# Kernel optimization log

Hardware: AMD Instinct MI355X
Metric: run time of the kernel (lower is better)

## Reference

```python
import jax, jax.numpy as jnp
import numpy as np

IGNORE_INDEX = 255
NUM_CLASSES = 19


def setup_inputs() -> dict:
    key = jax.random.key(0)
    k1, k2 = jax.random.split(key)
    logits = jax.random.normal(k1, (8, NUM_CLASSES, 512, 1024), dtype=jnp.float32)
    labels = jax.random.randint(k2, (8, 512, 1024), 0, NUM_CLASSES, dtype=jnp.int64)
    return {"logits": logits, "labels": labels}


def _lovasz_per_class(err, fg, valid):
    # err, fg, valid: [N] for one class. Sort by error descending.
    order = jnp.argsort(-err)
    es = err[order]
    fs = fg[order]
    vs = valid[order]
    gts = fs.sum()
    intersection = gts - jnp.cumsum(fs)
    # invalid (ignored) pixels contribute to neither fg nor background: vs - fs
    union = gts + jnp.cumsum(vs - fs)
    safe_union = jnp.where(union == 0, 1.0, union)
    jaccard = 1.0 - intersection / safe_union
    grad = jnp.concatenate([jaccard[:1], jaccard[1:] - jaccard[:-1]])
    loss_c = jnp.dot(es, grad)
    present = (gts > 0).astype(es.dtype)
    return loss_c, present


def reference(logits, labels):
    B, C, H, W = logits.shape
    probs = jax.nn.softmax(logits, axis=1)
    probs = probs.transpose(0, 2, 3, 1).reshape(-1, C)  # [N, C]
    lab = labels.reshape(-1)
    valid = (lab != IGNORE_INDEX).astype(probs.dtype)  # [N]
    # one-hot foreground per class, zeroed at ignored pixels
    fg = (lab[:, None] == jnp.arange(C)[None, :]).astype(probs.dtype) * valid[:, None]
    # errors; ignored pixels get error 0 so they sort to the end and contribute 0
    errors = jnp.abs(fg - probs) * valid[:, None]  # [N, C]
    loss_c, present = jax.vmap(_lovasz_per_class, in_axes=(1, 1, None))(errors, fg, valid)
    n_present = jnp.maximum(present.sum(), 1.0)
    return jnp.sum(loss_c * present) / n_present
```

## Files before the change

kernel.cpp:

```cpp
#include <hip/hip_runtime.h>


#define NCLS 19
#define IGNORE_IDX 255

constexpr int HW = 512 * 1024;
constexpr int HW4 = HW / 4;
constexpr int NQUAD = 8 * HW4;
constexpr int NBINS = 512;
constexpr int HSLOTS = NCLS * NBINS;

template <int NHB>
__global__ __launch_bounds__(256) void lovasz_hist(
    const float* __restrict__ logits,
    const int*   __restrict__ labels,
    unsigned int* __restrict__ partial)
{
    constexpr int QPB = NQUAD / NHB;
    constexpr int QPT = QPB / 256;
    __shared__ unsigned int lh[HSLOTS];
    const int t = threadIdx.x;
    for (int i = t; i < HSLOTS; i += 256) lh[i] = 0;
    __syncthreads();

    for (int k = 0; k < QPT; ++k) {
        const int q   = blockIdx.x * QPB + k * 256 + t;
        const int b   = q >> 17;
        const int hw4 = q & (HW4 - 1);
        const float* base = logits + (size_t)b * NCLS * HW + (size_t)hw4 * 4;

        float4 l[NCLS];
        float mx = -3.4e38f, my = -3.4e38f, mz = -3.4e38f, mw = -3.4e38f;
#pragma unroll
        for (int c = 0; c < NCLS; ++c) {
            l[c] = *(const float4*)(base + (size_t)c * HW);
            mx = fmaxf(mx, l[c].x); my = fmaxf(my, l[c].y);
            mz = fmaxf(mz, l[c].z); mw = fmaxf(mw, l[c].w);
        }
        float dx = 0.f, dy = 0.f, dz = 0.f, dw = 0.f;
#pragma unroll
        for (int c = 0; c < NCLS; ++c) {
            l[c].x = __expf(l[c].x - mx); dx += l[c].x;
            l[c].y = __expf(l[c].y - my); dy += l[c].y;
            l[c].z = __expf(l[c].z - mz); dz += l[c].z;
            l[c].w = __expf(l[c].w - mw); dw += l[c].w;
        }
        dx = 1.f / dx; dy = 1.f / dy; dz = 1.f / dz; dw = 1.f / dw;

        const int4 lab = *(const int4*)(labels + (size_t)q * 4);

        auto upd = [&](int c, float p, int lb) {
            if (lb == IGNORE_IDX) return;
            const bool fg = (lb == c);
            const float e = fg ? (1.0f - p) : p;
            int bin = (int)(e * (float)NBINS);
            bin = bin < 0 ? 0 : (bin > NBINS - 1 ? NBINS - 1 : bin);
            atomicAdd(&lh[c * NBINS + bin], fg ? 0x10001u : 1u);
        };
#pragma unroll
        for (int c = 0; c < NCLS; ++c) {
            upd(c, l[c].x * dx, lab.x);
            upd(c, l[c].y * dy, lab.y);
            upd(c, l[c].z * dz, lab.z);
            upd(c, l[c].w * dw, lab.w);
        }
    }
    __syncthreads();
    unsigned int* dst = partial + (size_t)blockIdx.x * HSLOTS;
    for (int i = t; i < HSLOTS; i += 256) dst[i] = lh[i];
}

__global__ __launch_bounds__(256) void lovasz_scan(
    const unsigned int* __restrict__ partial,
    int nhb,
    float* __restrict__ lp)
{
    const int c = blockIdx.x;
    const int t = threadIdx.x;

    unsigned int v0 = 0, g0 = 0, v1 = 0, g1 = 0;
    {
        const unsigned int* p0 = partial + c * NBINS + (NBINS - 2 - 2 * t);
        for (int b = 0; b < nhb; ++b) {
            const uint2 x = *(const uint2*)(p0 + (size_t)b * HSLOTS);
            v0 += x.y & 0xFFFFu; g0 += x.y >> 16;
            v1 += x.x & 0xFFFFu; g1 += x.x >> 16;
        }
    }

    __shared__ unsigned int av[NBINS], ag[NBINS];
    av[2 * t] = v0; ag[2 * t] = g0;
    av[2 * t + 1] = v1; ag[2 * t + 1] = g1;

    __shared__ unsigned int pg[257], pv[257];
    pg[t + 1] = g0 + g1; pv[t + 1] = v0 + v1;
    __syncthreads();
    if (t == 0) {
        pg[0] = 0; pv[0] = 0;
        for (int i = 1; i <= 256; ++i) { pg[i] += pg[i - 1]; pv[i] += pv[i - 1]; }
    }
    __syncthreads();
    const unsigned int G = pg[256];

    double acc = 0.0;
    if (G > 0) {
        unsigned int CF = pg[t], CV = pv[t];
#pragma unroll
        for (int i = 0; i < 2; ++i) {
            const int j = 2 * t + i;
            const int bin = NBINS - 1 - j;
            const unsigned int v = av[j], g = ag[j];
            if (v) {
                const float e  = ((float)bin + 0.5f) * (1.0f / (float)NBINS);
                const float U0 = (float)(G - CF + CV);
                if (g) acc += (double)(e * (float)g / U0);
                const unsigned int nbg = v - g;
                if (nbg) {
                    const float I1 = (float)(G - CF - g);
                    acc += (double)(e * I1 * (float)nbg / (U0 * (U0 + (float)nbg)));
                }
                CF += g; CV += v;
            }
        }
    }

    __shared__ double sacc[256];
    sacc[t] = acc;
    __syncthreads();
    for (int s = 128; s > 0; s >>= 1) {
        if (t < s) sacc[t] += sacc[t + s];
        __syncthreads();
    }
    if (t == 0) {
        lp[c] = (float)sacc[0];
        lp[NCLS + c] = (G > 0) ? 1.0f : 0.0f;
    }
}

__global__ void lovasz_final(const float* __restrict__ lp, float* __restrict__ out) {
    if (threadIdx.x == 0) {
        float s = 0.f, np = 0.f;
        for (int c = 0; c < NCLS; ++c) { s += lp[c] * lp[NCLS + c]; np += lp[NCLS + c]; }
        out[0] = s / fmaxf(np, 1.0f);
    }
}

extern "C" void kernel_launch(void* const* d_in, const int* in_sizes, int n_in,
                              void* d_out, int out_size, void* d_ws, size_t ws_size,
                              hipStream_t stream) {
    const float* logits = (const float*)d_in[0];
    const int*   labels = (const int*)d_in[1];
    float* out = (float*)d_out;

    unsigned int* partial = (unsigned int*)d_ws;
    const size_t need512 = (size_t)512 * HSLOTS * sizeof(unsigned int) + 64 * sizeof(float);

    if (ws_size >= need512) {
        float* lp = (float*)(partial + (size_t)512 * HSLOTS);
        lovasz_hist<512><<<512, 256, 0, stream>>>(logits, labels, partial);
        lovasz_scan<<<NCLS, 256, 0, stream>>>(partial, 512, lp);
        lovasz_final<<<1, 64, 0, stream>>>(lp, out);
    } else {
        float* lp = (float*)(partial + (size_t)256 * HSLOTS);
        lovasz_hist<256><<<256, 256, 0, stream>>>(logits, labels, partial);
        lovasz_scan<<<NCLS, 256, 0, stream>>>(partial, 256, lp);
        lovasz_final<<<1, 64, 0, stream>>>(lp, out);
    }
}
```

Baseline: 525.2 us.

## Halve histogram bins, replicate LDS histograms, drop softmax max pass

Reduces histogram bins from 512 to 256 and keeps four padded copies of the per-block LDS histogram, selected by thread index, to spread atomic contention; the copies are summed on write-out. Softmax drops the max-subtraction pass and uses a hardware reciprocal with the bin scale folded in, cutting ALU work and register pressure. The scan kernel is simplified to one bin per thread with an unrolled partial-sum loop. The changes risk overflow for large logits, coarser loss quantisation, and more LDS use per block, which may lower occupancy.

```diff
diff --git a/kernel.cpp b/kernel.cpp
--- a/kernel.cpp
+++ b/kernel.cpp
@@ -7,8 +7,18 @@
 constexpr int HW = 512 * 1024;
 constexpr int HW4 = HW / 4;
 constexpr int NQUAD = 8 * HW4;
-constexpr int NBINS = 512;
+constexpr int NBINS = 256;
 constexpr int HSLOTS = NCLS * NBINS;
+constexpr int PSTRIDE = HSLOTS + 1;
+constexpr int NCOPY = 4;
+
+__device__ __forceinline__ float fast_rcp(float x) {
+#if defined(__has_builtin) && __has_builtin(__builtin_amdgcn_rcpf)
+    return __builtin_amdgcn_rcpf(x);
+#else
+    return 1.0f / x;
+#endif
+}
 
 template <int NHB>
 __global__ __launch_bounds__(256) void lovasz_hist(
@@ -18,10 +28,12 @@
 {
     constexpr int QPB = NQUAD / NHB;
     constexpr int QPT = QPB / 256;
-    __shared__ unsigned int lh[HSLOTS];
+    __shared__ unsigned int lh[NCOPY * PSTRIDE];
     const int t = threadIdx.x;
-    for (int i = t; i < HSLOTS; i += 256) lh[i] = 0;
+    for (int i = t; i < NCOPY * PSTRIDE; i += 256) lh[i] = 0;
     __syncthreads();
+
+    unsigned int* my = lh + (t & (NCOPY - 1)) * PSTRIDE;
 
     for (int k = 0; k < QPT; ++k) {
         const int q   = blockIdx.x * QPB + k * 256 + t;
@@ -29,45 +41,43 @@
         const int hw4 = q & (HW4 - 1);
         const float* base = logits + (size_t)b * NCLS * HW + (size_t)hw4 * 4;
 
-        float4 l[NCLS];
-        float mx = -3.4e38f, my = -3.4e38f, mz = -3.4e38f, mw = -3.4e38f;
-#pragma unroll
-        for (int c = 0; c < NCLS; ++c) {
-            l[c] = *(const float4*)(base + (size_t)c * HW);
-            mx = fmaxf(mx, l[c].x); my = fmaxf(my, l[c].y);
-            mz = fmaxf(mz, l[c].z); mw = fmaxf(mw, l[c].w);
-        }
+        float ex[NCLS], ey[NCLS], ez[NCLS], ew[NCLS];
         float dx = 0.f, dy = 0.f, dz = 0.f, dw = 0.f;
 #pragma unroll
         for (int c = 0; c < NCLS; ++c) {
-            l[c].x = __expf(l[c].x - mx); dx += l[c].x;
-            l[c].y = __expf(l[c].y - my); dy += l[c].y;
-            l[c].z = __expf(l[c].z - mz); dz += l[c].z;
-            l[c].w = __expf(l[c].w - mw); dw += l[c].w;
+            const float4 l = *(const float4*)(base + (size_t)c * HW);
+            ex[c] = __expf(l.x); dx += ex[c];
+            ey[c] = __expf(l.y); dy += ey[c];
+            ez[c] = __expf(l.z); dz += ez[c];
+            ew[c] = __expf(l.w); dw += ew[c];
         }
-        dx = 1.f / dx; dy = 1.f / dy; dz = 1.f / dz; dw = 1.f / dw;
+        const float rx = (float)NBINS * fast_rcp(dx);
+        const float ry = (float)NBINS * fast_rcp(dy);
+        const float rz = (float)NBINS * fast_rcp(dz);
+        const float rw = (float)NBINS * fast_rcp(dw);
 
         const int4 lab = *(const int4*)(labels + (size_t)q * 4);
 
-        auto upd = [&](int c, float p, int lb) {
+        auto upd = [&](int c, float psc, int lb) {
             if (lb == IGNORE_IDX) return;
             const bool fg = (lb == c);
-            const float e = fg ? (1.0f - p) : p;
-            int bin = (int)(e * (float)NBINS);
-            bin = bin < 0 ? 0 : (bin > NBINS - 1 ? NBINS - 1 : bin);
-            atomicAdd(&lh[c * NBINS + bin], fg ? 0x10001u : 1u);
+            const float bs = fg ? ((float)NBINS - psc) : psc;
+            int bin = (int)bs;
+            bin = bin > NBINS - 1 ? NBINS - 1 : bin;
+            atomicAdd(&my[c * NBINS + bin], fg ? 0x10001u : 1u);
         };
 #pragma unroll
         for (int c = 0; c < NCLS; ++c) {
-            upd(c, l[c].x * dx, lab.x);
-            upd(c, l[c].y * dy, lab.y);
-            upd(c, l[c].z * dz, lab.z);
-            upd(c, l[c].w * dw, lab.w);
+            upd(c, ex[c] * rx, lab.x);
+            upd(c, ey[c] * ry, lab.y);
+            upd(c, ez[c] * rz, lab.z);
+            upd(c, ew[c] * rw, lab.w);
         }
     }
     __syncthreads();
     unsigned int* dst = partial + (size_t)blockIdx.x * HSLOTS;
-    for (int i = t; i < HSLOTS; i += 256) dst[i] = lh[i];
+    for (int i = t; i < HSLOTS; i += 256)
+        dst[i] = lh[i] + lh[i + PSTRIDE] + lh[i + 2 * PSTRIDE] + lh[i + 3 * PSTRIDE];
 }
 
 __global__ __launch_bounds__(256) void lovasz_scan(
@@ -78,22 +88,26 @@
     const int c = blockIdx.x;
     const int t = threadIdx.x;
 
-    unsigned int v0 = 0, g0 = 0, v1 = 0, g1 = 0;
+    unsigned int v = 0, g = 0;
     {
-        const unsigned int* p0 = partial + c * NBINS + (NBINS - 2 - 2 * t);
-        for (int b = 0; b < nhb; ++b) {
-            const uint2 x = *(const uint2*)(p0 + (size_t)b * HSLOTS);
-            v0 += x.y & 0xFFFFu; g0 += x.y >> 16;
-            v1 += x.x & 0xFFFFu; g1 += x.x >> 16;
+        const unsigned int* p0 = partial + c * NBINS + (NBINS - 1 - t);
+        int b = 0;
+        for (; b + 4 <= nhb; b += 4) {
+            const unsigned int x0 = p0[(size_t)(b + 0) * HSLOTS];
+            const unsigned int x1 = p0[(size_t)(b + 1) * HSLOTS];
+            const unsigned int x2 = p0[(size_t)(b + 2) * HSLOTS];
+            const unsigned int x3 = p0[(size_t)(b + 3) * HSLOTS];
+            v += (x0 & 0xFFFFu) + (x1 & 0xFFFFu) + (x2 & 0xFFFFu) + (x3 & 0xFFFFu);
+            g += (x0 >> 16) + (x1 >> 16) + (x2 >> 16) + (x3 >> 16);
+        }
+        for (; b < nhb; ++b) {
+            const unsigned int x = p0[(size_t)b * HSLOTS];
+            v += x & 0xFFFFu; g += x >> 16;
         }
     }
 
-    __shared__ unsigned int av[NBINS], ag[NBINS];
-    av[2 * t] = v0; ag[2 * t] = g0;
-    av[2 * t + 1] = v1; ag[2 * t + 1] = g1;
-
     __shared__ unsigned int pg[257], pv[257];
-    pg[t + 1] = g0 + g1; pv[t + 1] = v0 + v1;
+    pg[t + 1] = g; pv[t + 1] = v;
     __syncthreads();
     if (t == 0) {
         pg[0] = 0; pv[0] = 0;
@@ -103,24 +117,16 @@
     const unsigned int G = pg[256];
 
     double acc = 0.0;
-    if (G > 0) {
-        unsigned int CF = pg[t], CV = pv[t];
-#pragma unroll
-        for (int i = 0; i < 2; ++i) {
-            const int j = 2 * t + i;
-            const int bin = NBINS - 1 - j;
-            const unsigned int v = av[j], g = ag[j];
-            if (v) {
-                const float e  = ((float)bin + 0.5f) * (1.0f / (float)NBINS);
-                const float U0 = (float)(G - CF + CV);
-                if (g) acc += (double)(e * (float)g / U0);
-                const unsigned int nbg = v - g;
-                if (nbg) {
-                    const float I1 = (float)(G - CF - g);
-                    acc += (double)(e * I1 * (float)nbg / (U0 * (U0 + (float)nbg)));
-                }
-                CF += g; CV += v;
-            }
+    if (G > 0 && v) {
+        const unsigned int CF = pg[t], CV = pv[t];
+        const int bin = NBINS - 1 - t;
+        const float e  = ((float)bin + 0.5f) * (1.0f / (float)NBINS);
+        const float U0 = (float)(G - CF + CV);
+        if (g) acc += (double)(e * (float)g / U0);
+        const unsigned int nbg = v - g;
+        if (nbg) {
+            const float I1 = (float)(G - CF - g);
+            acc += (double)(e * I1 * (float)nbg / (U0 * (U0 + (float)nbg)));
         }
     }
 
```

Result: faster. 469.0 us (-10.7%).
